# Kernel optimization log

Hardware: AMD Instinct MI355X
Metric: run time of the kernel (lower is better)

## Reference

```python
import jax, jax.numpy as jnp
import numpy as np

H, C = 3, 64          # heads, out_channels
NEG_SLOPE = 0.2       # PyG GATConv leaky_relu default
LN_EPS = 1e-5


def setup_inputs() -> dict:
    key = jax.random.key(0)
    ks = jax.random.split(key, 20)
    N, E, D_in, edge_dim = 50000, 800000, 64, 5
    g = lambda k, shape: (jax.random.normal(k, shape, dtype=jnp.float32) * 0.1)
    return {
        "x": jax.random.normal(ks[0], (N, D_in), dtype=jnp.float32),
        "edge_attr": jax.random.normal(ks[1], (E, edge_dim), dtype=jnp.float32),
        "lin_w": g(ks[2], (D_in, H * C)),          # GATConv.lin (bias=False)
        "att_src": g(ks[3], (H, C)),
        "att_dst": g(ks[4], (H, C)),
        "lin_edge_w": g(ks[5], (edge_dim, H * C)),  # GATConv.lin_edge (bias=False)
        "att_edge": g(ks[6], (H, C)),
        "gat_bias": jnp.zeros((H * C,), jnp.float32),
        "w1": g(ks[7], (H * C, C)),
        "b1": jnp.zeros((C,), jnp.float32),
        "ln1_g": jnp.ones((C,), jnp.float32),
        "ln1_b": jnp.zeros((C,), jnp.float32),
        "w2": g(ks[8], (C, C)),
        "b2": jnp.zeros((C,), jnp.float32),
        "ln2_g": jnp.ones((C,), jnp.float32),
        "ln2_b": jnp.zeros((C,), jnp.float32),
        "edge_index": jax.random.randint(ks[9], (2, E), 0, N),
    }


def layer_norm(x, g, b):
    m = jnp.mean(x, axis=-1, keepdims=True)
    v = jnp.mean((x - m) ** 2, axis=-1, keepdims=True)
    return (x - m) * jax.lax.rsqrt(v + LN_EPS) * g + b


def gat_conv(x, edge_index, edge_attr, lin_w, att_src, att_dst,
             lin_edge_w, att_edge, gat_bias):
    N = x.shape[0]
    src, dst = edge_index[0], edge_index[1]

    # add_self_loops=True with fill_value='mean': self-loop edge_attr is the
    # per-node mean of incoming edge attributes (0 if node has no in-edges).
    attr_sum = jax.ops.segment_sum(edge_attr, dst, num_segments=N)       # [N, edge_dim]
    cnt = jax.ops.segment_sum(jnp.ones((dst.shape[0],), edge_attr.dtype), dst, num_segments=N)
    loop_attr = attr_sum / jnp.maximum(cnt, 1.0)[:, None]
    loop = jnp.arange(N, dtype=src.dtype)
    src = jnp.concatenate([src, loop])
    dst = jnp.concatenate([dst, loop])
    ea = jnp.concatenate([edge_attr, loop_attr], axis=0)                  # [E2, edge_dim]

    xs = (x @ lin_w).reshape(N, H, C)                                     # [N, H, C]
    a_src = jnp.einsum('nhc,hc->nh', xs, att_src)                         # [N, H]
    a_dst = jnp.einsum('nhc,hc->nh', xs, att_dst)                         # [N, H]
    e = (ea @ lin_edge_w).reshape(-1, H, C)                               # [E2, H, C]
    a_edge = jnp.einsum('ehc,hc->eh', e, att_edge)                        # [E2, H]

    logits = a_src[src] + a_dst[dst] + a_edge                             # [E2, H]
    logits = jnp.where(logits >= 0, logits, NEG_SLOPE * logits)           # leaky_relu

    # segment softmax over incoming edges of each dst node (self loops ensure non-empty)
    lmax = jax.ops.segment_max(logits, dst, num_segments=N)               # [N, H]
    ex = jnp.exp(logits - lmax[dst])
    denom = jax.ops.segment_sum(ex, dst, num_segments=N)                  # [N, H]
    alpha = ex / denom[dst]                                               # [E2, H]

    msgs = alpha[:, :, None] * xs[src]                                    # [E2, H, C]
    out = jax.ops.segment_sum(msgs, dst, num_segments=N)                  # [N, H, C]
    return out.reshape(N, H * C) + gat_bias


def reference(x, edge_attr, lin_w, att_src, att_dst, lin_edge_w, att_edge,
              gat_bias, w1, b1, ln1_g, ln1_b, w2, b2, ln2_g, ln2_b, edge_index):
    x_gat = gat_conv(x, edge_index, edge_attr, lin_w, att_src, att_dst,
                     lin_edge_w, att_edge, gat_bias)
    x_gat = x_gat @ w1 + b1                         # linear1: [N, C]
    x_gat = layer_norm(x + x_gat, ln1_g, ln1_b)     # layerNorm1(x + x_gat)
    lin = x_gat @ w2 + b2                           # linear2
    out = layer_norm(lin + x_gat, ln2_g, ln2_b)     # layerNorm2(lin + x_gat)
    return out                                      # dropout p=0 -> identity
```

## Files before the change

kernel.cpp:

```cpp
#include <hip/hip_runtime.h>


#define HH 3
#define CC 64
#define DIN 64
#define ED 5
#define HC 192
#define NEG_SLOPE 0.2f
#define LN_EPS 1e-5f
#define LOG2E 1.44269504f

typedef __attribute__((ext_vector_type(8))) short bf16x8;
typedef __attribute__((ext_vector_type(4))) float f32x4;

__device__ __forceinline__ float leaky(float l) { return (l >= 0.f) ? l : NEG_SLOPE * l; }

__device__ __forceinline__ unsigned short f2bf(float f) {
    unsigned u = __float_as_uint(f);
    unsigned r = (u + 0x7FFFu + ((u >> 16) & 1u)) >> 16;
    return (unsigned short)r;
}
__device__ __forceinline__ float bf2f(unsigned short u) {
    return __uint_as_float((unsigned)u << 16);
}
__device__ __forceinline__ float bf_lo(unsigned v) { return __uint_as_float(v << 16); }
__device__ __forceinline__ float bf_hi(unsigned v) { return __uint_as_float(v & 0xFFFF0000u); }

__device__ __forceinline__ bf16x8 pack8(float4 a, float4 b) {
    bf16x8 r;
    r[0] = (short)f2bf(a.x); r[1] = (short)f2bf(a.y);
    r[2] = (short)f2bf(a.z); r[3] = (short)f2bf(a.w);
    r[4] = (short)f2bf(b.x); r[5] = (short)f2bf(b.y);
    r[6] = (short)f2bf(b.z); r[7] = (short)f2bf(b.w);
    return r;
}

#define PREP_TOT (HC*DIN + DIN*HC + CC*CC + CC + ED*HH)
#define PREP_BLOCKS 30
__global__ __launch_bounds__(256) void k_prep_cnt(const float* __restrict__ lin_w,
                                                  const float* __restrict__ w1,
                                                  const float* __restrict__ w2,
                                                  const float* __restrict__ b1,
                                                  const float* __restrict__ gat_bias,
                                                  const float* __restrict__ lin_edge_w,
                                                  const float* __restrict__ att_edge,
                                                  unsigned short* __restrict__ linwt,
                                                  unsigned short* __restrict__ w1t,
                                                  unsigned short* __restrict__ w2t,
                                                  float* __restrict__ b1p,
                                                  float* __restrict__ we,
                                                  const int* __restrict__ ei,
                                                  int* __restrict__ icnt, int E) {
    if (blockIdx.x < PREP_BLOCKS) {
        for (int i = blockIdx.x * 256 + threadIdx.x; i < PREP_TOT; i += PREP_BLOCKS * 256) {
            if (i < HC * DIN) {
                int c = i >> 6, k = i & 63;
                linwt[i] = f2bf(lin_w[k * HC + c]);
            } else if (i < 2 * HC * DIN) {
                int j = i - HC * DIN;
                int c = j / HC, k = j - c * HC;
                w1t[j] = f2bf(w1[k * CC + c]);
            } else if (i < 2 * HC * DIN + CC * CC) {
                int j = i - 2 * HC * DIN;
                int c = j >> 6, k = j & 63;
                w2t[j] = f2bf(w2[k * CC + c]);
            } else if (i < 2 * HC * DIN + CC * CC + CC) {
                int c = i - (2 * HC * DIN + CC * CC);
                float s = b1[c];
                for (int k = 0; k < HC; ++k) s += gat_bias[k] * w1[k * CC + c];
                b1p[c] = s;
            } else {
                int q = i - (2 * HC * DIN + CC * CC + CC);
                int d = q / HH, h = q - d * HH;
                float s = 0.f;
                for (int c = 0; c < CC; ++c)
                    s += lin_edge_w[d * HC + h * CC + c] * att_edge[h * CC + c];
                we[q] = s * LOG2E;
            }
        }
    } else {
        int nb = gridDim.x - PREP_BLOCKS;
        for (int e = (blockIdx.x - PREP_BLOCKS) * 256 + threadIdx.x; e < E; e += nb * 256)
            atomicAdd(&icnt[ei[E + e]], 1);
    }
}

__global__ __launch_bounds__(256) void k_xs(const float* __restrict__ x,
                                            const unsigned short* __restrict__ linwt,
                                            const float* __restrict__ att_src,
                                            const float* __restrict__ att_dst,
                                            unsigned short* __restrict__ xsb,
                                            float* __restrict__ a_src,
                                            float* __restrict__ a_dst, int N) {
    int lane = threadIdx.x & 63, w = threadIdx.x >> 6;
    int l15 = lane & 15, kg = (lane >> 4) * 8;
    int nb = blockIdx.x * 64;
    int arow = nb + w * 16 + l15;
    int arow_c = min(arow, N - 1);

    f32x4 acc[12];
    #pragma unroll
    for (int ct = 0; ct < 12; ++ct) acc[ct] = (f32x4){0.f, 0.f, 0.f, 0.f};

    #pragma unroll
    for (int k0 = 0; k0 < DIN; k0 += 32) {
        const float* ap = x + (size_t)arow_c * DIN + k0 + kg;
        float4 a0 = *(const float4*)ap;
        float4 a1 = *(const float4*)(ap + 4);
        bf16x8 af = pack8(a0, a1);
        #pragma unroll
        for (int ct = 0; ct < 12; ++ct) {
            bf16x8 bf = *(const bf16x8*)(linwt + (size_t)(ct * 16 + l15) * DIN + k0 + kg);
            acc[ct] = __builtin_amdgcn_mfma_f32_16x16x32_bf16(af, bf, acc[ct], 0, 0, 0);
        }
    }

    float asv[12], adv[12];
    #pragma unroll
    for (int ct = 0; ct < 12; ++ct) {
        int c = ct * 16 + l15;
        asv[ct] = att_src[c]; adv[ct] = att_dst[c];
    }

    int rbase = nb + w * 16 + (lane >> 4) * 4;
    #pragma unroll
    for (int j = 0; j < 4; ++j) {
        int r = rbase + j;
        bool ok = r < N;
        float ps0 = 0.f, ps1 = 0.f, ps2 = 0.f, pd0 = 0.f, pd1 = 0.f, pd2 = 0.f;
        #pragma unroll
        for (int ct = 0; ct < 12; ++ct) {
            float v = acc[ct][j];
            if (ok) xsb[(size_t)r * HC + ct * 16 + l15] = f2bf(v);
            float s = v * asv[ct], d = v * adv[ct];
            if (ct < 4)      { ps0 += s; pd0 += d; }
            else if (ct < 8) { ps1 += s; pd1 += d; }
            else             { ps2 += s; pd2 += d; }
        }
        #pragma unroll
        for (int o = 1; o < 16; o <<= 1) {
            ps0 += __shfl_xor(ps0, o, 64); pd0 += __shfl_xor(pd0, o, 64);
            ps1 += __shfl_xor(ps1, o, 64); pd1 += __shfl_xor(pd1, o, 64);
            ps2 += __shfl_xor(ps2, o, 64); pd2 += __shfl_xor(pd2, o, 64);
        }
        if (ok && l15 == 0) {
            a_src[r * HH + 0] = ps0 * LOG2E; a_src[r * HH + 1] = ps1 * LOG2E;
            a_src[r * HH + 2] = ps2 * LOG2E;
            a_dst[r * HH + 0] = pd0 * LOG2E; a_dst[r * HH + 1] = pd1 * LOG2E;
            a_dst[r * HH + 2] = pd2 * LOG2E;
        }
    }
}

__global__ __launch_bounds__(256) void k_scan1(const int* __restrict__ icnt,
                                               int* __restrict__ bsum, int N) {
    int i = blockIdx.x * 256 + threadIdx.x;
    int lane = threadIdx.x & 63, wid = threadIdx.x >> 6;
    int v = (i < N) ? icnt[i] : 0;
    #pragma unroll
    for (int o = 32; o; o >>= 1) v += __shfl_xor(v, o, 64);
    __shared__ int wt[4];
    if (lane == 0) wt[wid] = v;
    __syncthreads();
    if (threadIdx.x == 0) bsum[blockIdx.x] = wt[0] + wt[1] + wt[2] + wt[3];
}

__global__ __launch_bounds__(1024) void k_scan2(const int* __restrict__ bsum,
                                                int* __restrict__ boff, int nb) {
    __shared__ int s[1024];
    int t = threadIdx.x;
    int v = (t < nb) ? bsum[t] : 0;
    s[t] = v;
    __syncthreads();
    for (int d = 1; d < 1024; d <<= 1) {
        int u = (t >= d) ? s[t - d] : 0;
        __syncthreads();
        s[t] += u;
        __syncthreads();
    }
    if (t < nb) boff[t] = s[t] - v;
}

__global__ __launch_bounds__(256) void k_scan3(const int* __restrict__ icnt,
                                               const int* __restrict__ boff,
                                               int* __restrict__ off,
                                               int* __restrict__ cursor, int N) {
    int i = blockIdx.x * 256 + threadIdx.x;
    int lane = threadIdx.x & 63, wid = threadIdx.x >> 6;
    int v = (i < N) ? icnt[i] : 0;
    int incl = v;
    #pragma unroll
    for (int o = 1; o < 64; o <<= 1) {
        int u = __shfl_up(incl, o, 64);
        if (lane >= o) incl += u;
    }
    __shared__ int wt[4];
    if (lane == 63) wt[wid] = incl;
    __syncthreads();
    int wpre = 0;
    for (int w = 0; w < wid; ++w) wpre += wt[w];
    int excl = boff[blockIdx.x] + wpre + incl - v;
    if (i < N) {
        off[i] = excl;
        cursor[i] = excl;
        if (i == N - 1) off[N] = excl + v;
    }
}

__global__ __launch_bounds__(256) void k_fill(const float* __restrict__ ea,
                                              const int* __restrict__ ei,
                                              const float* __restrict__ a_src,
                                              const float* __restrict__ we,
                                              int* __restrict__ cursor,
                                              uint4* __restrict__ payload, int E) {
    int e = blockIdx.x * blockDim.x + threadIdx.x;
    if (e >= E) return;
    int s = ei[e], d = ei[E + e];
    float attr[ED];
    #pragma unroll
    for (int j = 0; j < ED; ++j) attr[j] = ea[(size_t)e * ED + j];
    float aeh[HH], lp[HH];
    #pragma unroll
    for (int h = 0; h < HH; ++h) {
        float a = 0.f;
        #pragma unroll
        for (int j = 0; j < ED; ++j) a += attr[j] * we[j * HH + h];
        aeh[h] = a;
        lp[h] = a_src[s * HH + h] + a;
    }
    int pos = atomicAdd(&cursor[d], 1);
    uint4 pk;
    pk.x = (unsigned)f2bf(lp[0])  | ((unsigned)f2bf(lp[1])  << 16);
    pk.y = (unsigned)f2bf(lp[2])  | ((unsigned)f2bf(aeh[0]) << 16);
    pk.z = (unsigned)f2bf(aeh[1]) | ((unsigned)f2bf(aeh[2]) << 16);
    pk.w = (unsigned)s;
    payload[pos] = pk;
}

__global__ __launch_bounds__(256) void k_gat(const unsigned short* __restrict__ xsb,
                                             const float* __restrict__ a_src,
                                             const float* __restrict__ a_dst,
                                             const int* __restrict__ off,
                                             const uint4* __restrict__ payload,
                                             unsigned short* __restrict__ oaccb, int N) {
    __shared__ float4 wbuf[4][64];
    int lane = threadIdx.x & 63;
    int wid  = threadIdx.x >> 6;
    for (int n = blockIdx.x * 4 + wid; n < N; n += gridDim.x * 4) {
        int beg = off[n], end = off[n + 1];
        int deg = end - beg;
        float ad0 = a_dst[n * HH + 0], ad1 = a_dst[n * HH + 1], ad2 = a_dst[n * HH + 2];
        float asl0 = a_src[n * HH + 0], asl1 = a_src[n * HH + 1], asl2 = a_src[n * HH + 2];
        unsigned nb_ = (unsigned)n * HC + lane;
        float xn0 = bf2f(xsb[nb_]), xn1 = bf2f(xsb[nb_ + 64]), xn2 = bf2f(xsb[nb_ + 128]);

        float pden0 = 0.f, pden1 = 0.f, pden2 = 0.f;
        float pae0 = 0.f, pae1 = 0.f, pae2 = 0.f;
        float a0A = 0.f, a1A = 0.f, a2A = 0.f;
        float a0B = 0.f, a1B = 0.f, a2B = 0.f;

        for (int c0 = 0; c0 < deg; c0 += 64) {
            int cn = min(deg - c0, 64);
            float w0 = 0.f, w1 = 0.f, w2 = 0.f;
            int src = 0;
            if (lane < cn) {
                uint4 p = payload[beg + c0 + lane];
                w0 = exp2f(leaky(bf_lo(p.x) + ad0));
                w1 = exp2f(leaky(bf_hi(p.x) + ad1));
                w2 = exp2f(leaky(bf_lo(p.y) + ad2));
                pae0 += bf_hi(p.y);
                pae1 += bf_lo(p.z);
                pae2 += bf_hi(p.z);
                pden0 += w0; pden1 += w1; pden2 += w2;
                src = (int)p.w;
            }
            wbuf[wid][lane] = make_float4(w0, w1, w2, __int_as_float(src));
            int i = 0;
            for (; i + 2 <= cn; i += 2) {
                float4 ta = wbuf[wid][i];
                float4 tb = wbuf[wid][i + 1];
                unsigned sa = (unsigned)__float_as_int(ta.w) * HC + lane;
                unsigned sb = (unsigned)__float_as_int(tb.w) * HC + lane;
                a0A += ta.x * bf2f(xsb[sa]);
                a1A += ta.y * bf2f(xsb[sa + 64]);
                a2A += ta.z * bf2f(xsb[sa + 128]);
                a0B += tb.x * bf2f(xsb[sb]);
                a1B += tb.y * bf2f(xsb[sb + 64]);
                a2B += tb.z * bf2f(xsb[sb + 128]);
            }
            if (i < cn) {
                float4 ta = wbuf[wid][i];
                unsigned sa = (unsigned)__float_as_int(ta.w) * HC + lane;
                a0A += ta.x * bf2f(xsb[sa]);
                a1A += ta.y * bf2f(xsb[sa + 64]);
                a2A += ta.z * bf2f(xsb[sa + 128]);
            }
        }

        #pragma unroll
        for (int o = 32; o; o >>= 1) {
            pden0 += __shfl_xor(pden0, o, 64);
            pden1 += __shfl_xor(pden1, o, 64);
            pden2 += __shfl_xor(pden2, o, 64);
            pae0  += __shfl_xor(pae0, o, 64);
            pae1  += __shfl_xor(pae1, o, 64);
            pae2  += __shfl_xor(pae2, o, 64);
        }

        float dc = fmaxf((float)deg, 1.0f);
        float inv_dc = 1.0f / dc;
        float sl0 = leaky(asl0 + ad0 + pae0 * inv_dc);
        float sl1 = leaky(asl1 + ad1 + pae1 * inv_dc);
        float sl2 = leaky(asl2 + ad2 + pae2 * inv_dc);
        float e0 = exp2f(sl0), e1 = exp2f(sl1), e2 = exp2f(sl2);
        float den0 = pden0 + e0, den1 = pden1 + e1, den2 = pden2 + e2;
        float acc0 = a0A + a0B + e0 * xn0;
        float acc1 = a1A + a1B + e1 * xn1;
        float acc2 = a2A + a2B + e2 * xn2;
        size_t nbse = (size_t)n * HC;
        oaccb[nbse + 0 * CC + lane] = f2bf(acc0 / den0);
        oaccb[nbse + 1 * CC + lane] = f2bf(acc1 / den1);
        oaccb[nbse + 2 * CC + lane] = f2bf(acc2 / den2);
    }
}

__global__ __launch_bounds__(256) void k_mlp(const unsigned short* __restrict__ oaccb,
                                             const unsigned short* __restrict__ w1t,
                                             const unsigned short* __restrict__ w2t,
                                             const float* __restrict__ b1p,
                                             const float* __restrict__ x,
                                             const float* __restrict__ g1,
                                             const float* __restrict__ be1,
                                             const float* __restrict__ b2,
                                             const float* __restrict__ g2,
                                             const float* __restrict__ be2,
                                             float* __restrict__ out, int N) {
    __shared__ unsigned short H1[64 * 72];
    int lane = threadIdx.x & 63, w = threadIdx.x >> 6;
    int l15 = lane & 15, kg = (lane >> 4) * 8;
    int nb = blockIdx.x * 64;
    int arow = nb + w * 16 + l15;
    int arow_c = min(arow, N - 1);

    float c_b1[4], c_g1[4], c_be1[4], c_b2[4], c_g2[4], c_be2[4];
    #pragma unroll
    for (int ct = 0; ct < 4; ++ct) {
        int c = ct * 16 + l15;
        c_b1[ct] = b1p[c]; c_g1[ct] = g1[c]; c_be1[ct] = be1[c];
        c_b2[ct] = b2[c];  c_g2[ct] = g2[c]; c_be2[ct] = be2[c];
    }

    f32x4 acc[4];
    #pragma unroll
    for (int ct = 0; ct < 4; ++ct) acc[ct] = (f32x4){0.f, 0.f, 0.f, 0.f};
    #pragma unroll
    for (int k0 = 0; k0 < HC; k0 += 32) {
        bf16x8 af = *(const bf16x8*)(oaccb + (size_t)arow_c * HC + k0 + kg);
        #pragma unroll
        for (int ct = 0; ct < 4; ++ct) {
            bf16x8 bf = *(const bf16x8*)(w1t + (size_t)(ct * 16 + l15) * HC + k0 + kg);
            acc[ct] = __builtin_amdgcn_mfma_f32_16x16x32_bf16(af, bf, acc[ct], 0, 0, 0);
        }
    }

    int rbase = nb + w * 16 + (lane >> 4) * 4;
    int rloc0 = w * 16 + (lane >> 4) * 4;
    float h1v[4][4];
    float y[4][4];
    #pragma unroll
    for (int j = 0; j < 4; ++j) {
        int r = min(rbase + j, N - 1);
        #pragma unroll
        for (int ct = 0; ct < 4; ++ct)
            y[ct][j] = acc[ct][j] + c_b1[ct] + x[(size_t)r * DIN + ct * 16 + l15];
    }
    #pragma unroll
    for (int j = 0; j < 4; ++j) {
        float s = y[0][j] + y[1][j] + y[2][j] + y[3][j];
        #pragma unroll
        for (int o = 1; o < 16; o <<= 1) s += __shfl_xor(s, o, 64);
        float m = s * (1.0f / CC);
        float vs = 0.f;
        #pragma unroll
        for (int ct = 0; ct < 4; ++ct) { float d = y[ct][j] - m; vs += d * d; }
        #pragma unroll
        for (int o = 1; o < 16; o <<= 1) vs += __shfl_xor(vs, o, 64);
        float inv = rsqrtf(vs * (1.0f / CC) + LN_EPS);
        #pragma unroll
        for (int ct = 0; ct < 4; ++ct) {
            float h = (y[ct][j] - m) * inv * c_g1[ct] + c_be1[ct];
            h1v[ct][j] = h;
            H1[(rloc0 + j) * 72 + ct * 16 + l15] = f2bf(h);
        }
    }
    __syncthreads();

    f32x4 acc2[4];
    #pragma unroll
    for (int ct = 0; ct < 4; ++ct) acc2[ct] = (f32x4){0.f, 0.f, 0.f, 0.f};
    #pragma unroll
    for (int k0 = 0; k0 < CC; k0 += 32) {
        bf16x8 af = *(const bf16x8*)&H1[(w * 16 + l15) * 72 + k0 + kg];
        #pragma unroll
        for (int ct = 0; ct < 4; ++ct) {
            bf16x8 bf = *(const bf16x8*)(w2t + (size_t)(ct * 16 + l15) * CC + k0 + kg);
            acc2[ct] = __builtin_amdgcn_mfma_f32_16x16x32_bf16(af, bf, acc2[ct], 0, 0, 0);
        }
    }

    #pragma unroll
    for (int j = 0; j < 4; ++j) {
        float z0 = acc2[0][j] + c_b2[0] + h1v[0][j];
        float z1 = acc2[1][j] + c_b2[1] + h1v[1][j];
        float z2 = acc2[2][j] + c_b2[2] + h1v[2][j];
        float z3 = acc2[3][j] + c_b2[3] + h1v[3][j];
        float s = z0 + z1 + z2 + z3;
        #pragma unroll
        for (int o = 1; o < 16; o <<= 1) s += __shfl_xor(s, o, 64);
        float m = s * (1.0f / CC);
        float d0 = z0 - m, d1 = z1 - m, d2 = z2 - m, d3 = z3 - m;
        float vs = d0 * d0 + d1 * d1 + d2 * d2 + d3 * d3;
        #pragma unroll
        for (int o = 1; o < 16; o <<= 1) vs += __shfl_xor(vs, o, 64);
        float inv = rsqrtf(vs * (1.0f / CC) + LN_EPS);
        int r = rbase + j;
        if (r < N) {
            out[(size_t)r * CC + 0 * 16 + l15] = d0 * inv * c_g2[0] + c_be2[0];
            out[(size_t)r * CC + 1 * 16 + l15] = d1 * inv * c_g2[1] + c_be2[1];
            out[(size_t)r * CC + 2 * 16 + l15] = d2 * inv * c_g2[2] + c_be2[2];
            out[(size_t)r * CC + 3 * 16 + l15] = d3 * inv * c_g2[3] + c_be2[3];
        }
    }
}

extern "C" void kernel_launch(void* const* d_in, const int* in_sizes, int n_in,
                              void* d_out, int out_size, void* d_ws, size_t ws_size,
                              hipStream_t stream) {
    const float* x          = (const float*)d_in[0];
    const float* edge_attr  = (const float*)d_in[1];
    const float* lin_w      = (const float*)d_in[2];
    const float* att_src    = (const float*)d_in[3];
    const float* att_dst    = (const float*)d_in[4];
    const float* lin_edge_w = (const float*)d_in[5];
    const float* att_edge   = (const float*)d_in[6];
    const float* gat_bias   = (const float*)d_in[7];
    const float* w1         = (const float*)d_in[8];
    const float* b1         = (const float*)d_in[9];
    const float* ln1_g      = (const float*)d_in[10];
    const float* ln1_b      = (const float*)d_in[11];
    const float* w2         = (const float*)d_in[12];
    const float* b2         = (const float*)d_in[13];
    const float* ln2_g      = (const float*)d_in[14];
    const float* ln2_b      = (const float*)d_in[15];
    const int*   ei         = (const int*)d_in[16];
    float* out = (float*)d_out;

    const int N = in_sizes[0] / DIN;
    const int E = in_sizes[1] / ED;
    const int nb_scan = (N + 255) / 256;

    char* ws = (char*)d_ws;
    size_t off_b = 0;
    auto alloc = [&](size_t bytes) {
        size_t o = off_b;
        off_b = (off_b + bytes + 255) & ~(size_t)255;
        return o;
    };
    int* icnt = (int*)(ws + alloc((size_t)N * 4));
    size_t zero_bytes = off_b;
    unsigned short* xsb   = (unsigned short*)(ws + alloc((size_t)N * HC * 2));
    unsigned short* oaccb = (unsigned short*)(ws + alloc((size_t)N * HC * 2));
    float*  a_srcb  = (float*)(ws + alloc((size_t)N * HH * 4));
    float*  a_dstb  = (float*)(ws + alloc((size_t)N * HH * 4));
    int*    offb    = (int*)(ws + alloc((size_t)(N + 1) * 4));
    int*    cursor  = (int*)(ws + alloc((size_t)N * 4));
    int*    bsum    = (int*)(ws + alloc((size_t)nb_scan * 4));
    int*    boff    = (int*)(ws + alloc((size_t)nb_scan * 4));
    uint4*  payload = (uint4*)(ws + alloc((size_t)E * 16));
    unsigned short* linwt = (unsigned short*)(ws + alloc((size_t)HC * DIN * 2));
    unsigned short* w1t   = (unsigned short*)(ws + alloc((size_t)DIN * HC * 2));
    unsigned short* w2t   = (unsigned short*)(ws + alloc((size_t)CC * CC * 2));
    float* b1p = (float*)(ws + alloc((size_t)CC * 4));
    float* we  = (float*)(ws + alloc((size_t)ED * HH * 4));
    (void)ws_size; (void)n_in; (void)out_size;

    hipMemsetAsync(d_ws, 0, zero_bytes, stream);

    k_prep_cnt<<<PREP_BLOCKS + (E + 255) / 256, 256, 0, stream>>>(
        lin_w, w1, w2, b1, gat_bias, lin_edge_w, att_edge,
        linwt, w1t, w2t, b1p, we, ei, icnt, E);
    k_xs<<<(N + 63) / 64, 256, 0, stream>>>(x, linwt, att_src, att_dst, xsb, a_srcb, a_dstb, N);
    k_scan1<<<nb_scan, 256, 0, stream>>>(icnt, bsum, N);
    k_scan2<<<1, 1024, 0, stream>>>(bsum, boff, nb_scan);
    k_scan3<<<nb_scan, 256, 0, stream>>>(icnt, boff, offb, cursor, N);
    k_fill<<<(E + 255) / 256, 256, 0, stream>>>(edge_attr, ei, a_srcb, we, cursor,
                                                payload, E);
    k_gat<<<(N + 3) / 4, 256, 0, stream>>>(xsb, a_srcb, a_dstb, offb, payload, oaccb, N);
    k_mlp<<<(N + 63) / 64, 256, 0, stream>>>(oaccb, w1t, w2t, b1p, x,
                                             ln1_g, ln1_b, b2, ln2_g, ln2_b, out, N);
}
```

Baseline: 198.3 us.

## Interleave heads 0/1 in xs rows and fold a_dst into edge payload

```diff
diff --git a/kernel.cpp b/kernel.cpp
--- a/kernel.cpp
+++ b/kernel.cpp
@@ -13,7 +13,7 @@
 typedef __attribute__((ext_vector_type(8))) short bf16x8;
 typedef __attribute__((ext_vector_type(4))) float f32x4;
 
-__device__ __forceinline__ float leaky(float l) { return (l >= 0.f) ? l : NEG_SLOPE * l; }
+__device__ __forceinline__ float leaky(float l) { return fmaxf(l, NEG_SLOPE * l); }
 
 __device__ __forceinline__ unsigned short f2bf(float f) {
     unsigned u = __float_as_uint(f);
@@ -131,11 +131,19 @@
         #pragma unroll
         for (int ct = 0; ct < 12; ++ct) {
             float v = acc[ct][j];
-            if (ok) xsb[(size_t)r * HC + ct * 16 + l15] = f2bf(v);
             float s = v * asv[ct], d = v * adv[ct];
             if (ct < 4)      { ps0 += s; pd0 += d; }
             else if (ct < 8) { ps1 += s; pd1 += d; }
             else             { ps2 += s; pd2 += d; }
+        }
+        if (ok) {
+            unsigned* row32 = (unsigned*)(xsb + (size_t)r * HC);
+            #pragma unroll
+            for (int ct = 0; ct < 4; ++ct) {
+                int c = ct * 16 + l15;
+                row32[c] = (unsigned)f2bf(acc[ct][j]) | ((unsigned)f2bf(acc[ct + 4][j]) << 16);
+                xsb[(size_t)r * HC + 128 + c] = f2bf(acc[ct + 8][j]);
+            }
         }
         #pragma unroll
         for (int o = 1; o < 16; o <<= 1) {
@@ -210,6 +218,7 @@
 __global__ __launch_bounds__(256) void k_fill(const float* __restrict__ ea,
                                               const int* __restrict__ ei,
                                               const float* __restrict__ a_src,
+                                              const float* __restrict__ a_dst,
                                               const float* __restrict__ we,
                                               int* __restrict__ cursor,
                                               uint4* __restrict__ payload, int E) {
@@ -226,7 +235,7 @@
         #pragma unroll
         for (int j = 0; j < ED; ++j) a += attr[j] * we[j * HH + h];
         aeh[h] = a;
-        lp[h] = a_src[s * HH + h] + a;
+        lp[h] = a_src[s * HH + h] + a_dst[d * HH + h] + a;
     }
     int pos = atomicAdd(&cursor[d], 1);
     uint4 pk;
@@ -246,13 +255,11 @@
     __shared__ float4 wbuf[4][64];
     int lane = threadIdx.x & 63;
     int wid  = threadIdx.x >> 6;
+    const unsigned* xs32 = (const unsigned*)xsb;
+    unsigned c128ml = 128u - (unsigned)lane;
     for (int n = blockIdx.x * 4 + wid; n < N; n += gridDim.x * 4) {
         int beg = off[n], end = off[n + 1];
         int deg = end - beg;
-        float ad0 = a_dst[n * HH + 0], ad1 = a_dst[n * HH + 1], ad2 = a_dst[n * HH + 2];
-        float asl0 = a_src[n * HH + 0], asl1 = a_src[n * HH + 1], asl2 = a_src[n * HH + 2];
-        unsigned nb_ = (unsigned)n * HC + lane;
-        float xn0 = bf2f(xsb[nb_]), xn1 = bf2f(xsb[nb_ + 64]), xn2 = bf2f(xsb[nb_ + 128]);
 
         float pden0 = 0.f, pden1 = 0.f, pden2 = 0.f;
         float pae0 = 0.f, pae1 = 0.f, pae2 = 0.f;
@@ -265,9 +272,9 @@
             int src = 0;
             if (lane < cn) {
                 uint4 p = payload[beg + c0 + lane];
-                w0 = exp2f(leaky(bf_lo(p.x) + ad0));
-                w1 = exp2f(leaky(bf_hi(p.x) + ad1));
-                w2 = exp2f(leaky(bf_lo(p.y) + ad2));
+                w0 = exp2f(leaky(bf_lo(p.x)));
+                w1 = exp2f(leaky(bf_hi(p.x)));
+                w2 = exp2f(leaky(bf_lo(p.y)));
                 pae0 += bf_hi(p.y);
                 pae1 += bf_lo(p.z);
                 pae2 += bf_hi(p.z);
@@ -279,21 +286,22 @@
             for (; i + 2 <= cn; i += 2) {
                 float4 ta = wbuf[wid][i];
                 float4 tb = wbuf[wid][i + 1];
-                unsigned sa = (unsigned)__float_as_int(ta.w) * HC + lane;
-                unsigned sb = (unsigned)__float_as_int(tb.w) * HC + lane;
-                a0A += ta.x * bf2f(xsb[sa]);
-                a1A += ta.y * bf2f(xsb[sa + 64]);
-                a2A += ta.z * bf2f(xsb[sa + 128]);
-                a0B += tb.x * bf2f(xsb[sb]);
-                a1B += tb.y * bf2f(xsb[sb + 64]);
-                a2B += tb.z * bf2f(xsb[sb + 128]);
+                unsigned ia = __umul24((unsigned)__float_as_int(ta.w), 96u) + lane;
+                unsigned ib = __umul24((unsigned)__float_as_int(tb.w), 96u) + lane;
+                unsigned va = xs32[ia];
+                unsigned vb = xs32[ib];
+                float xa2 = bf2f(xsb[(ia << 1) + c128ml]);
+                float xb2 = bf2f(xsb[(ib << 1) + c128ml]);
+                a0A += ta.x * bf_lo(va); a1A += ta.y * bf_hi(va); a2A += ta.z * xa2;
+                a0B += tb.x * bf_lo(vb); a1B += tb.y * bf_hi(vb); a2B += tb.z * xb2;
             }
             if (i < cn) {
                 float4 ta = wbuf[wid][i];
-                unsigned sa = (unsigned)__float_as_int(ta.w) * HC + lane;
-                a0A += ta.x * bf2f(xsb[sa]);
-                a1A += ta.y * bf2f(xsb[sa + 64]);
-                a2A += ta.z * bf2f(xsb[sa + 128]);
+                unsigned ia = __umul24((unsigned)__float_as_int(ta.w), 96u) + lane;
+                unsigned va = xs32[ia];
+                a0A += ta.x * bf_lo(va);
+                a1A += ta.y * bf_hi(va);
+                a2A += ta.z * bf2f(xsb[(ia << 1) + c128ml]);
             }
         }
 
@@ -308,19 +316,24 @@
         }
 
         float dc = fmaxf((float)deg, 1.0f);
-        float inv_dc = 1.0f / dc;
-        float sl0 = leaky(asl0 + ad0 + pae0 * inv_dc);
-        float sl1 = leaky(asl1 + ad1 + pae1 * inv_dc);
-        float sl2 = leaky(asl2 + ad2 + pae2 * inv_dc);
+        float inv_dc = __builtin_amdgcn_rcpf(dc);
+        float sl0 = leaky(a_src[n * HH + 0] + a_dst[n * HH + 0] + pae0 * inv_dc);
+        float sl1 = leaky(a_src[n * HH + 1] + a_dst[n * HH + 1] + pae1 * inv_dc);
+        float sl2 = leaky(a_src[n * HH + 2] + a_dst[n * HH + 2] + pae2 * inv_dc);
         float e0 = exp2f(sl0), e1 = exp2f(sl1), e2 = exp2f(sl2);
-        float den0 = pden0 + e0, den1 = pden1 + e1, den2 = pden2 + e2;
-        float acc0 = a0A + a0B + e0 * xn0;
-        float acc1 = a1A + a1B + e1 * xn1;
-        float acc2 = a2A + a2B + e2 * xn2;
+        unsigned ian = __umul24((unsigned)n, 96u) + lane;
+        unsigned van = xs32[ian];
+        float xn2 = bf2f(xsb[(ian << 1) + c128ml]);
+        float r0 = __builtin_amdgcn_rcpf(pden0 + e0);
+        float r1 = __builtin_amdgcn_rcpf(pden1 + e1);
+        float r2 = __builtin_amdgcn_rcpf(pden2 + e2);
+        float acc0 = (a0A + a0B + e0 * bf_lo(van)) * r0;
+        float acc1 = (a1A + a1B + e1 * bf_hi(van)) * r1;
+        float acc2 = (a2A + a2B + e2 * xn2) * r2;
         size_t nbse = (size_t)n * HC;
-        oaccb[nbse + 0 * CC + lane] = f2bf(acc0 / den0);
-        oaccb[nbse + 1 * CC + lane] = f2bf(acc1 / den1);
-        oaccb[nbse + 2 * CC + lane] = f2bf(acc2 / den2);
+        oaccb[nbse + 0 * CC + lane] = f2bf(acc0);
+        oaccb[nbse + 1 * CC + lane] = f2bf(acc1);
+        oaccb[nbse + 2 * CC + lane] = f2bf(acc2);
     }
 }
 
@@ -493,7 +506,7 @@
     k_scan1<<<nb_scan, 256, 0, stream>>>(icnt, bsum, N);
     k_scan2<<<1, 1024, 0, stream>>>(bsum, boff, nb_scan);
     k_scan3<<<nb_scan, 256, 0, stream>>>(icnt, boff, offb, cursor, N);
-    k_fill<<<(E + 255) / 256, 256, 0, stream>>>(edge_attr, ei, a_srcb, we, cursor,
+    k_fill<<<(E + 255) / 256, 256, 0, stream>>>(edge_attr, ei, a_srcb, a_dstb, we, cursor,
                                                 payload, E);
     k_gat<<<(N + 3) / 4, 256, 0, stream>>>(xsb, a_srcb, a_dstb, offb, payload, oaccb, N);
     k_mlp<<<(N + 63) / 64, 256, 0, stream>>>(oaccb, w1t, w2t, b1p, x,
```

Measured after the change: 192.1 us. 1.03x faster.
